# Performance work log

Measured on AMD Instinct MI355X. Metric: run time of the kernel, lower is better.

The kernel has to match this reference:

```python
import jax, jax.numpy as jnp
import numpy as np

D_MODEL = 1024
NHEAD = 16
D_K = D_MODEL // NHEAD
B, S = 4, 2048
LN_EPS = 1e-5


def setup_inputs() -> dict:
    key = jax.random.key(0)
    ks = jax.random.split(key, 12)
    sd = 1.0 / np.sqrt(D_MODEL)
    inp = {
        'x': jax.random.normal(ks[0], (B, S, D_MODEL), dtype=jnp.float32),
        'wq': jax.random.normal(ks[1], (D_MODEL, D_MODEL), dtype=jnp.float32) * sd,
        'bq': jnp.zeros((D_MODEL,), dtype=jnp.float32),
        'wk': jax.random.normal(ks[2], (D_MODEL, D_MODEL), dtype=jnp.float32) * sd,
        'bk': jnp.zeros((D_MODEL,), dtype=jnp.float32),
        'wv': jax.random.normal(ks[3], (D_MODEL, D_MODEL), dtype=jnp.float32) * sd,
        'bv': jnp.zeros((D_MODEL,), dtype=jnp.float32),
        'wo': jax.random.normal(ks[4], (D_MODEL, D_MODEL), dtype=jnp.float32) * sd,
        'bo': jnp.zeros((D_MODEL,), dtype=jnp.float32),
        'conv_w': jax.random.normal(ks[5], (D_MODEL, 3), dtype=jnp.float32) * (1.0 / np.sqrt(3.0)),
        'conv_b': jnp.zeros((D_MODEL,), dtype=jnp.float32),
        'ln_g': jnp.ones((D_MODEL,), dtype=jnp.float32),
        'ln_b': jnp.zeros((D_MODEL,), dtype=jnp.float32),
    }
    return inp


def _forward(x, wq, bq, wk, bk, wv, bv, wo, bo, conv_w, conv_b, ln_g, ln_b):
    b, s, d = x.shape
    # QKV projections -> [B, H, S, Dk]
    q = (x @ wq.T + bq).reshape(b, s, NHEAD, D_K).transpose(0, 2, 1, 3)
    k = (x @ wk.T + bk).reshape(b, s, NHEAD, D_K).transpose(0, 2, 1, 3)
    v = (x @ wv.T + bv).reshape(b, s, NHEAD, D_K).transpose(0, 2, 1, 3)
    # full attention, materialized scores [B, H, S, S]
    scores = jnp.einsum('bhqd,bhkd->bhqk', q, k) / jnp.sqrt(jnp.float32(D_K))
    attn = jax.nn.softmax(scores, axis=-1)  # dropout is identity in eval
    ctx = jnp.einsum('bhqk,bhkd->bhqd', attn, v)
    ctx = ctx.transpose(0, 2, 1, 3).reshape(b, s, d)
    global_attn = ctx @ wo.T + bo
    # depthwise conv1d, kernel 3, padding 1 along sequence
    xp = jnp.pad(x, ((0, 0), (1, 1), (0, 0)))
    local_attn = (xp[:, :-2] * conv_w[:, 0]
                  + xp[:, 1:-1] * conv_w[:, 1]
                  + xp[:, 2:] * conv_w[:, 2]
                  + conv_b)
    combined = global_attn + 0.3 * local_attn
    y = x + combined  # dropout identity in eval
    mu = jnp.mean(y, axis=-1, keepdims=True)
    var = jnp.mean(jnp.square(y - mu), axis=-1, keepdims=True)
    return (y - mu) * jax.lax.rsqrt(var + LN_EPS) * ln_g + ln_b


def reference(x, wq, bq, wk, bk, wv, bv, wo, bo, conv_w, conv_b, ln_g, ln_b):
    return _forward(x, wq, bq, wk, bk, wv, bv, wo, bo, conv_w, conv_b, ln_g, ln_b)
```

## Files before the change

### kernel.cpp

```cpp
#include <hip/hip_runtime.h>

#define DEV __device__ __forceinline__

typedef unsigned short u16;
typedef unsigned int u32;
using f32x4  = __attribute__((ext_vector_type(4))) float;
using f32x16 = __attribute__((ext_vector_type(16))) float;
using s16x8  = __attribute__((ext_vector_type(8))) short;
using u32x2  = __attribute__((ext_vector_type(2))) u32;
using u32x4  = __attribute__((ext_vector_type(4))) u32;
typedef int i32x2 __attribute__((ext_vector_type(2)));

#if __has_builtin(__builtin_amdgcn_exp2f)
#define EXP2(x) __builtin_amdgcn_exp2f(x)
#else
#define EXP2(x) exp2f(x)
#endif

__constant__ const float C2_SCALE = 0.18033688011112042f;
#define S2_SHIFT 17.312340490667560f

DEV u16 f2b(float f) {
  union { float f; u32 u; } v; v.f = f;
  return (u16)((v.u + 0x7FFFu + ((v.u >> 16) & 1u)) >> 16);
}
DEV float b2f(u16 u) {
  union { u32 u; float f; } v; v.u = ((u32)u) << 16;
  return v.f;
}

DEV u32 cvtpk(float lo, float hi) {
  u32 r;
  asm("v_cvt_pk_bf16_f32 %0, %1, %2" : "=v"(r) : "v"(lo), "v"(hi));
  return r;
}

#if __has_builtin(__builtin_amdgcn_permlane32_swap)
DEV void lane32_swap(u32& x, u32& y) {
  i32x2 r = __builtin_amdgcn_permlane32_swap((int)x, (int)y, false, false);
  x = (u32)r[0]; y = (u32)r[1];
}
#else
DEV void lane32_swap(u32& x, u32& y) {
  u32 xo = (u32)__shfl_xor((int)x, 32, 64);
  u32 yo = (u32)__shfl_xor((int)y, 32, 64);
  int hi = (int)((threadIdx.x & 63) >> 5);
  u32 nx = hi ? yo : x;
  u32 ny = hi ? y : xo;
  x = nx; y = ny;
}
#endif

DEV void gload16(const void* g, void* l) {
  __builtin_amdgcn_global_load_lds(
      (const __attribute__((address_space(1))) void*)g,
      (__attribute__((address_space(3))) void*)l, 16, 0, 0);
}

__global__ __launch_bounds__(256) void k_cvt(const float* __restrict__ src,
                                             u16* __restrict__ dst, int n4) {
  int i = blockIdx.x * 256 + threadIdx.x;
  if (i >= n4) return;
  float4 v = ((const float4*)src)[i];
  ushort4 o;
  o.x = f2b(v.x); o.y = f2b(v.y); o.z = f2b(v.z); o.w = f2b(v.w);
  ((ushort4*)dst)[i] = o;
}

__global__ __launch_bounds__(256) void k_cvt_w(
    const float* __restrict__ s0, const float* __restrict__ s1,
    const float* __restrict__ s2, const float* __restrict__ s3,
    u16* __restrict__ dst) {
  int blk = blockIdx.x;
  int widx = blk >> 10;
  int i = (blk & 1023) * 256 + threadIdx.x;
  const float* src = widx == 0 ? s0 : widx == 1 ? s1 : widx == 2 ? s2 : s3;
  float4 v = ((const float4*)src)[i];
  ushort4 o;
  o.x = f2b(v.x); o.y = f2b(v.y); o.z = f2b(v.z); o.w = f2b(v.w);
  ((ushort4*)(dst + (size_t)widx * 1048576))[i] = o;
}

template <int MODE>
__global__ __launch_bounds__(256) void k_gemm_bt(
    const u16* __restrict__ A, const u16* __restrict__ Bw,
    const float* __restrict__ bias0, const float* __restrict__ bias1,
    u16* __restrict__ C, int M, int N, int K) {
  __shared__ alignas(16) u16 lds_[16384];
  char* lds = (char*)lds_;
  const int t = threadIdx.x;
  const int wave = t >> 6, lane = t & 63;
  const int g = lane >> 4, fr = lane & 15;
  const int wr = (wave >> 1) * 64, wc = (wave & 1) * 64;
  const int m0 = blockIdx.y * 128, n0 = blockIdx.x * 128;
  const int chunk = t & 3;

  auto stage = [&](int k0, int buf) {
#pragma unroll
    for (int r = 0; r < 2; ++r) {
      int row = r * 64 + (t >> 2);
      int sw = 8 * (chunk ^ ((row >> 1) & 3));
      char* dst = lds + buf * 16384 + r * 4096 + wave * 1024;
      gload16(A  + (size_t)(m0 + row) * K + k0 + sw, dst);
      gload16(Bw + (size_t)(n0 + row) * K + k0 + sw, dst + 8192);
    }
  };

  f32x4 acc[4][4];
#pragma unroll
  for (int i = 0; i < 4; ++i)
#pragma unroll
    for (int j = 0; j < 4; ++j)
#pragma unroll
      for (int r = 0; r < 4; ++r) acc[i][j][r] = 0.f;

  const int nk = K >> 5;
  stage(0, 0);
  __syncthreads();
  for (int kt = 0; kt < nk; ++kt) {
    const int cur = kt & 1;
    if (kt + 1 < nk) stage((kt + 1) << 5, cur ^ 1);
    s16x8 af[4], bf4[4];
#pragma unroll
    for (int i = 0; i < 4; ++i) {
      int row = wr + i * 16 + fr;
      af[i] = *(const s16x8*)(lds + cur * 16384 + row * 64 +
                              ((g * 16) ^ ((((row >> 1) & 3)) << 4)));
    }
#pragma unroll
    for (int j = 0; j < 4; ++j) {
      int row = wc + j * 16 + fr;
      bf4[j] = *(const s16x8*)(lds + cur * 16384 + 8192 + row * 64 +
                               ((g * 16) ^ ((((row >> 1) & 3)) << 4)));
    }
    __builtin_amdgcn_s_setprio(1);
#pragma unroll
    for (int i = 0; i < 4; ++i)
#pragma unroll
      for (int j = 0; j < 4; ++j)
        acc[i][j] = __builtin_amdgcn_mfma_f32_16x16x32_bf16(af[i], bf4[j], acc[i][j], 0, 0, 0);
    __builtin_amdgcn_s_setprio(0);
    __syncthreads();
  }
#pragma unroll
  for (int j = 0; j < 4; ++j) {
    const int coltile = n0 + wc + j * 16;
    float sc = 1.f;
    const float* bp = bias0;
    if constexpr (MODE == 2) {
      if (coltile >= 1024) { bp = bias1 - 1024; sc = C2_SCALE; }
    }
#pragma unroll
    for (int i = 0; i < 4; ++i)
#pragma unroll
      for (int r = 0; r < 4; ++r) {
        int row = m0 + wr + i * 16 + g * 4 + r;
        int col = coltile + fr;
        float v;
        if constexpr (MODE == 1) v = acc[i][j][r] + bias0[row];
        else                     v = (acc[i][j][r] + bp[col]) * sc;
        C[(size_t)row * N + col] = f2b(v);
      }
  }
}

__global__ __launch_bounds__(256, 2) void k_attn(
    const u16* __restrict__ qkb, const u16* __restrict__ vtb,
    u16* __restrict__ ctx) {
  __shared__ alignas(16) u16 smem_[16384];
  char* smem = (char*)smem_;
  const int bh = blockIdx.x;
  const int b = bh >> 4, h = bh & 15;
  const int qblk = blockIdx.y;
  const int t = threadIdx.x, w = t >> 6, lane = t & 63;
  const int l31 = lane & 31, hi = lane >> 5;
  const int hc = h * 64;
  const int q0 = qblk * 256 + w * 64;

  s16x8 qf[2][4];
#pragma unroll
  for (int s = 0; s < 2; ++s) {
    const u16* qrow = qkb + (size_t)(b * 2048 + q0 + s * 32 + l31) * 2048 + hc + hi * 8;
#pragma unroll
    for (int ks = 0; ks < 4; ++ks) qf[s][ks] = *(const s16x8*)(qrow + ks * 16);
  }

  const u16* kbase  = qkb + (size_t)(b * 2048) * 2048 + 1024 + hc;
  const u16* vtbase = vtb + (size_t)hc * 8192 + b * 2048;

  const int lrow = lane >> 3, seg = lane & 7;
  auto stage = [&](int kt, int buf) {
    const int k0 = kt * 64;
#pragma unroll
    for (int r = 0; r < 2; ++r) {
      int row = r * 32 + w * 8 + lrow;
      int sw = 8 * (seg ^ (row & 7));
      char* dst = smem + buf * 16384 + r * 4096 + w * 1024;
      gload16(kbase  + (size_t)(k0 + row) * 2048 + sw, dst);
      gload16(vtbase + (size_t)row * 8192 + k0 + sw, dst + 8192);
    }
  };

  f32x16 octx[2][2], ns2;
#pragma unroll
  for (int r = 0; r < 16; ++r) {
    octx[0][0][r] = 0.f; octx[0][1][r] = 0.f;
    octx[1][0][r] = 0.f; octx[1][1][r] = 0.f;
    ns2[r] = -S2_SHIFT;
  }
  float lrun[2] = {0.f, 0.f};

  stage(0, 0);
  __syncthreads();
  for (int kt = 0; kt < 32; ++kt) {
    const int cur = kt & 1;
    if (kt + 1 < 32) stage(kt + 1, cur ^ 1);

    f32x16 st[2][2];
    __builtin_amdgcn_s_setprio(1);
#pragma unroll
    for (int ks = 0; ks < 4; ++ks) {
#pragma unroll
      for (int tt = 0; tt < 2; ++tt) {
        int row = tt * 32 + l31;
        s16x8 kf = *(const s16x8*)(smem + cur * 16384 + row * 128 +
                                   ((ks * 32 + hi * 16) ^ ((row & 7) << 4)));
#pragma unroll
        for (int s = 0; s < 2; ++s)
          st[s][tt] = __builtin_amdgcn_mfma_f32_32x32x16_bf16(
              kf, qf[s][ks], ks == 0 ? ns2 : st[s][tt], 0, 0, 0);
      }
    }
    __builtin_amdgcn_s_setprio(0);

    s16x8 pf[2][4];
#pragma unroll
    for (int s = 0; s < 2; ++s) {
      float sm = 0.f;
#pragma unroll
      for (int ks = 0; ks < 4; ++ks) {
        const int tt = ks >> 1, base = (ks & 1) * 8;
        float e[8];
#pragma unroll
        for (int j = 0; j < 8; ++j) {
          e[j] = EXP2(st[s][tt][base + j]);
          sm += e[j];
        }
        u32 u0 = cvtpk(e[0], e[1]), u1 = cvtpk(e[2], e[3]);
        u32 v0 = cvtpk(e[4], e[5]), v1 = cvtpk(e[6], e[7]);
        lane32_swap(u0, v0);
        lane32_swap(u1, v1);
        u32x4 f; f[0] = u0; f[1] = u1; f[2] = v0; f[3] = v1;
        pf[s][ks] = __builtin_bit_cast(s16x8, f);
      }
      lrun[s] += sm;
    }

    __builtin_amdgcn_s_setprio(1);
#pragma unroll
    for (int dt = 0; dt < 2; ++dt)
#pragma unroll
      for (int ks = 0; ks < 4; ++ks) {
        int row = dt * 32 + l31;
        s16x8 vf = *(const s16x8*)(smem + cur * 16384 + 8192 + row * 128 +
                                   ((ks * 32 + hi * 16) ^ ((row & 7) << 4)));
        octx[0][dt] = __builtin_amdgcn_mfma_f32_32x32x16_bf16(vf, pf[0][ks], octx[0][dt], 0, 0, 0);
        octx[1][dt] = __builtin_amdgcn_mfma_f32_32x32x16_bf16(vf, pf[1][ks], octx[1][dt], 0, 0, 0);
      }
    __builtin_amdgcn_s_setprio(0);
    __syncthreads();
  }

  float linv[2];
#pragma unroll
  for (int s = 0; s < 2; ++s) {
    u32 ua = __builtin_bit_cast(u32, lrun[s]), va = ua;
    lane32_swap(ua, va);
    linv[s] = 1.0f / (__builtin_bit_cast(float, ua) + __builtin_bit_cast(float, va));
  }

#pragma unroll
  for (int s = 0; s < 2; ++s) {
    const int ql = w * 64 + s * 32 + l31;
#pragma unroll
    for (int dt = 0; dt < 2; ++dt)
#pragma unroll
      for (int rq = 0; rq < 4; ++rq) {
        int d0 = 8 * rq + 4 * hi + 32 * dt;
        u32x2 pk;
        pk[0] = cvtpk(octx[s][dt][4 * rq + 0] * linv[s], octx[s][dt][4 * rq + 1] * linv[s]);
        pk[1] = cvtpk(octx[s][dt][4 * rq + 2] * linv[s], octx[s][dt][4 * rq + 3] * linv[s]);
        *(u32x2*)(smem + ql * 128 + ((2 * d0) ^ ((ql & 7) << 4))) = pk;
      }
  }
  __syncthreads();
  {
    int qr = t;
    u16* dst = ctx + (size_t)(b * 2048 + qblk * 256 + qr) * 1024 + hc;
#pragma unroll
    for (int i = 0; i < 8; ++i) {
      s16x8 v = *(const s16x8*)(smem + qr * 128 + ((i * 16) ^ ((qr & 7) << 4)));
      *(s16x8*)(dst + i * 8) = v;
    }
  }
}

__global__ __launch_bounds__(256) void k_epi(
    const float* __restrict__ x, const u16* __restrict__ gab,
    const float* __restrict__ cw, const float* __restrict__ cb,
    const float* __restrict__ lg, const float* __restrict__ lb,
    float* __restrict__ out) {
  __shared__ float red[4];
  const int n = ((blockIdx.x & 7) << 10) | (blockIdx.x >> 3);
  const int s = n & 2047;
  const int t = threadIdx.x;
  const int d0 = t * 4;
  const float* xr = x + (size_t)n * 1024;

  float xc[4], xm[4], xp[4];
  { float4 v = *(const float4*)(xr + d0); xc[0]=v.x; xc[1]=v.y; xc[2]=v.z; xc[3]=v.w; }
  if (s > 0) { float4 v = *(const float4*)(xr - 1024 + d0); xm[0]=v.x; xm[1]=v.y; xm[2]=v.z; xm[3]=v.w; }
  else { xm[0]=xm[1]=xm[2]=xm[3]=0.f; }
  if (s < 2047) { float4 v = *(const float4*)(xr + 1024 + d0); xp[0]=v.x; xp[1]=v.y; xp[2]=v.z; xp[3]=v.w; }
  else { xp[0]=xp[1]=xp[2]=xp[3]=0.f; }
  ushort4 gv = *(const ushort4*)(gab + (size_t)n * 1024 + d0);
  float ga4[4] = { b2f(gv.x), b2f(gv.y), b2f(gv.z), b2f(gv.w) };

  float y[4];
#pragma unroll
  for (int i = 0; i < 4; ++i) {
    int d = d0 + i;
    float lo = xm[i] * cw[d * 3] + xc[i] * cw[d * 3 + 1] + xp[i] * cw[d * 3 + 2] + cb[d];
    y[i] = xc[i] + ga4[i] + 0.3f * lo;
  }

  float sm = y[0] + y[1] + y[2] + y[3];
#pragma unroll
  for (int off = 32; off >= 1; off >>= 1) sm += __shfl_xor(sm, off, 64);
  if ((t & 63) == 0) red[t >> 6] = sm;
  __syncthreads();
  float mu = (red[0] + red[1] + red[2] + red[3]) * (1.f / 1024.f);
  __syncthreads();

  float vs = 0.f;
#pragma unroll
  for (int i = 0; i < 4; ++i) { float dd = y[i] - mu; vs += dd * dd; }
#pragma unroll
  for (int off = 32; off >= 1; off >>= 1) vs += __shfl_xor(vs, off, 64);
  if ((t & 63) == 0) red[t >> 6] = vs;
  __syncthreads();
  float var = (red[0] + red[1] + red[2] + red[3]) * (1.f / 1024.f);
  float rs = rsqrtf(var + 1e-5f);
#pragma unroll
  for (int i = 0; i < 4; ++i) {
    int d = d0 + i;
    out[(size_t)n * 1024 + d] = (y[i] - mu) * rs * lg[d] + lb[d];
  }
}

extern "C" void kernel_launch(void* const* d_in, const int* in_sizes, int n_in,
                              void* d_out, int out_size, void* d_ws, size_t ws_size,
                              hipStream_t stream) {
  const float* x  = (const float*)d_in[0];
  const float* wq = (const float*)d_in[1];
  const float* bq = (const float*)d_in[2];
  const float* wk = (const float*)d_in[3];
  const float* bk = (const float*)d_in[4];
  const float* wv = (const float*)d_in[5];
  const float* bv = (const float*)d_in[6];
  const float* wo = (const float*)d_in[7];
  const float* bo = (const float*)d_in[8];
  const float* cw = (const float*)d_in[9];
  const float* cb = (const float*)d_in[10];
  const float* lg = (const float*)d_in[11];
  const float* lb = (const float*)d_in[12];
  float* out = (float*)d_out;

  char* ws = (char*)d_ws;
  const size_t MB = 1ull << 20;
  u16* xb  = (u16*)(ws + 0);
  u16* wqb = (u16*)(ws + 16 * MB);
  u16* wkb = (u16*)(ws + 18 * MB);
  u16* wvb = (u16*)(ws + 20 * MB);
  u16* wob = (u16*)(ws + 22 * MB);
  u16* qkb = (u16*)(ws + 24 * MB);
  u16* vtb = (u16*)(ws + 56 * MB);
  u16* ctx = xb;
  u16* gab = qkb;

  k_cvt<<<8192, 256, 0, stream>>>(x, xb, 2097152);
  k_cvt_w<<<4096, 256, 0, stream>>>(wq, wk, wv, wo, wqb);

  k_gemm_bt<2><<<dim3(16, 64), 256, 0, stream>>>(xb, wqb, bq, bk, qkb, 8192, 2048, 1024);
  k_gemm_bt<1><<<dim3(64, 8), 256, 0, stream>>>(wvb, xb, bv, nullptr, vtb, 1024, 8192, 1024);

  k_attn<<<dim3(64, 8), 256, 0, stream>>>(qkb, vtb, ctx);

  k_gemm_bt<0><<<dim3(8, 64), 256, 0, stream>>>(ctx, wob, bo, nullptr, gab, 8192, 1024, 1024);

  k_epi<<<8192, 256, 0, stream>>>(x, gab, cw, cb, lg, lb, out);
}
```

Before: 200.6 us.

## Add 256x256-tile 8-wave GEMM with chunked staging for fused QK projection

```diff
diff --git a/kernel.cpp b/kernel.cpp
--- a/kernel.cpp
+++ b/kernel.cpp
@@ -16,6 +16,10 @@
 #else
 #define EXP2(x) exp2f(x)
 #endif
+
+#define WAITV(N) asm volatile("s_waitcnt vmcnt(" #N ")" ::: "memory")
+#define LGKM0 do { asm volatile("s_waitcnt lgkmcnt(0)" ::: "memory"); \
+                   __builtin_amdgcn_sched_barrier(0); } while (0)
 
 __constant__ const float C2_SCALE = 0.18033688011112042f;
 #define S2_SHIFT 17.312340490667560f
@@ -81,11 +85,129 @@
   ((ushort4*)(dst + (size_t)widx * 1048576))[i] = o;
 }
 
+#define QUAD(QA, QB)                                                          \
+  do {                                                                        \
+    _Pragma("unroll")                                                         \
+    for (int kk = 0; kk < 2; ++kk)                                            \
+      _Pragma("unroll")                                                       \
+      for (int f = 0; f < 4; ++f)                                             \
+        _Pragma("unroll")                                                     \
+        for (int j = 0; j < 2; ++j)                                           \
+          acc[(QA)*4 + f][(QB)*2 + j] = __builtin_amdgcn_mfma_f32_16x16x32_bf16( \
+              af[f][kk], bf[(QB)*2 + j][kk], acc[(QA)*4 + f][(QB)*2 + j], 0, 0, 0); \
+  } while (0)
+
+__global__ __launch_bounds__(512, 2) void k_gemm8(
+    const u16* __restrict__ A, const u16* __restrict__ Bw,
+    const float* __restrict__ bq, const float* __restrict__ bk,
+    u16* __restrict__ C, int M, int N, int K) {
+  __shared__ alignas(16) u16 lds_[65536];
+  char* lds = (char*)lds_;
+  const int t = threadIdx.x;
+  const int wave = t >> 6, lane = t & 63;
+  const int g = lane >> 4, fr = lane & 15;
+  const int wm = wave >> 2, wn = wave & 3;
+  const int m0 = blockIdx.y * 256, n0 = blockIdx.x * 256;
+  const int seg = t & 7, trow = t >> 3;
+
+  auto stage_chunk = [&](int kt, int buf, int chunk) {
+    const int k0 = kt << 6;
+    const u16* src = (chunk < 2) ? A : Bw;
+    const int isB = chunk >> 1, half = chunk & 1;
+    const int gbase = (isB ? n0 : m0) + half * 128;
+    char* dbase = lds + buf * 65536 + isB * 32768 + half * 16384 + wave * 1024;
+#pragma unroll
+    for (int r = 0; r < 2; ++r) {
+      int rowc = r * 64 + trow;
+      gload16(src + (size_t)(gbase + rowc) * K + k0 + 8 * (seg ^ (rowc & 7)),
+              dbase + r * 8192);
+    }
+  };
+
+  f32x4 acc[8][4];
+#pragma unroll
+  for (int i = 0; i < 8; ++i)
+#pragma unroll
+    for (int j = 0; j < 4; ++j)
+#pragma unroll
+      for (int r = 0; r < 4; ++r) acc[i][j][r] = 0.f;
+
+  s16x8 af[4][2], bf[4][2];
+  const int nk = K >> 6;
+
+  stage_chunk(0, 0, 0); stage_chunk(0, 0, 1);
+  stage_chunk(0, 0, 2); stage_chunk(0, 0, 3);
+
+  for (int kt = 0; kt < nk; ++kt) {
+    const int cur = kt & 1, nxt = cur ^ 1;
+    const bool more = (kt + 1 < nk);
+    const char* ab = lds + cur * 65536;
+    const char* bb = lds + cur * 65536 + 32768;
+
+    auto lda = [&](int f, int kk) -> s16x8 {
+      int row = wm * 128 + f * 16 + fr;
+      return *(const s16x8*)(ab + row * 128 + ((kk * 64 + g * 16) ^ ((row & 7) << 4)));
+    };
+    auto ldb = [&](int j, int kk) -> s16x8 {
+      int row = wn * 64 + j * 16 + fr;
+      return *(const s16x8*)(bb + row * 128 + ((kk * 64 + g * 16) ^ ((row & 7) << 4)));
+    };
+
+    if (more) { stage_chunk(kt + 1, nxt, 0); WAITV(2); } else WAITV(0);
+    __builtin_amdgcn_s_barrier();
+    __builtin_amdgcn_sched_barrier(0);
+#pragma unroll
+    for (int f = 0; f < 4; ++f) { af[f][0] = lda(f, 0); af[f][1] = lda(f, 1); }
+#pragma unroll
+    for (int j = 0; j < 2; ++j) { bf[j][0] = ldb(j, 0); bf[j][1] = ldb(j, 1); }
+    LGKM0;
+    __builtin_amdgcn_s_setprio(1); QUAD(0, 0); __builtin_amdgcn_s_setprio(0);
+    __builtin_amdgcn_s_barrier();
+
+#pragma unroll
+    for (int j = 2; j < 4; ++j) { bf[j][0] = ldb(j, 0); bf[j][1] = ldb(j, 1); }
+    if (more) stage_chunk(kt + 1, nxt, 1);
+    __builtin_amdgcn_s_barrier();
+    LGKM0;
+    __builtin_amdgcn_s_setprio(1); QUAD(0, 1); __builtin_amdgcn_s_setprio(0);
+    __builtin_amdgcn_s_barrier();
+
+#pragma unroll
+    for (int f = 0; f < 4; ++f) { af[f][0] = lda(f + 4, 0); af[f][1] = lda(f + 4, 1); }
+    if (more) stage_chunk(kt + 1, nxt, 2);
+    __builtin_amdgcn_s_barrier();
+    LGKM0;
+    __builtin_amdgcn_s_setprio(1); QUAD(1, 1); __builtin_amdgcn_s_setprio(0);
+    __builtin_amdgcn_s_barrier();
+
+    if (more) stage_chunk(kt + 1, nxt, 3);
+    __builtin_amdgcn_s_barrier();
+    __builtin_amdgcn_s_setprio(1); QUAD(1, 0); __builtin_amdgcn_s_setprio(0);
+    __builtin_amdgcn_s_barrier();
+  }
+
+#pragma unroll
+  for (int j = 0; j < 4; ++j) {
+    const int coltile = n0 + wn * 64 + j * 16;
+    const bool isK = coltile >= 1024;
+    const float* bp = isK ? (bk - 1024) : bq;
+    const float sc = isK ? C2_SCALE : 1.f;
+#pragma unroll
+    for (int f = 0; f < 8; ++f)
+#pragma unroll
+      for (int r = 0; r < 4; ++r) {
+        int row = m0 + wm * 128 + f * 16 + g * 4 + r;
+        int col = coltile + fr;
+        C[(size_t)row * N + col] = f2b((acc[f][j][r] + bp[col]) * sc);
+      }
+  }
+}
+
 template <int MODE>
 __global__ __launch_bounds__(256) void k_gemm_bt(
     const u16* __restrict__ A, const u16* __restrict__ Bw,
-    const float* __restrict__ bias0, const float* __restrict__ bias1,
-    u16* __restrict__ C, int M, int N, int K) {
+    const float* __restrict__ bias0, u16* __restrict__ C,
+    int M, int N, int K) {
   __shared__ alignas(16) u16 lds_[16384];
   char* lds = (char*)lds_;
   const int t = threadIdx.x;
@@ -144,21 +266,13 @@
   }
 #pragma unroll
   for (int j = 0; j < 4; ++j) {
-    const int coltile = n0 + wc + j * 16;
-    float sc = 1.f;
-    const float* bp = bias0;
-    if constexpr (MODE == 2) {
-      if (coltile >= 1024) { bp = bias1 - 1024; sc = C2_SCALE; }
-    }
 #pragma unroll
     for (int i = 0; i < 4; ++i)
 #pragma unroll
       for (int r = 0; r < 4; ++r) {
         int row = m0 + wr + i * 16 + g * 4 + r;
-        int col = coltile + fr;
-        float v;
-        if constexpr (MODE == 1) v = acc[i][j][r] + bias0[row];
-        else                     v = (acc[i][j][r] + bp[col]) * sc;
+        int col = n0 + wc + j * 16 + fr;
+        float v = acc[i][j][r] + (MODE == 1 ? bias0[row] : bias0[col]);
         C[(size_t)row * N + col] = f2b(v);
       }
   }
@@ -380,7 +494,6 @@
   const size_t MB = 1ull << 20;
   u16* xb  = (u16*)(ws + 0);
   u16* wqb = (u16*)(ws + 16 * MB);
-  u16* wkb = (u16*)(ws + 18 * MB);
   u16* wvb = (u16*)(ws + 20 * MB);
   u16* wob = (u16*)(ws + 22 * MB);
   u16* qkb = (u16*)(ws + 24 * MB);
@@ -391,12 +504,12 @@
   k_cvt<<<8192, 256, 0, stream>>>(x, xb, 2097152);
   k_cvt_w<<<4096, 256, 0, stream>>>(wq, wk, wv, wo, wqb);
 
-  k_gemm_bt<2><<<dim3(16, 64), 256, 0, stream>>>(xb, wqb, bq, bk, qkb, 8192, 2048, 1024);
-  k_gemm_bt<1><<<dim3(64, 8), 256, 0, stream>>>(wvb, xb, bv, nullptr, vtb, 1024, 8192, 1024);
+  k_gemm8<<<dim3(8, 32), 512, 0, stream>>>(xb, wqb, bq, bk, qkb, 8192, 2048, 1024);
+  k_gemm_bt<1><<<dim3(64, 8), 256, 0, stream>>>(wvb, xb, bv, vtb, 1024, 8192, 1024);
 
   k_attn<<<dim3(64, 8), 256, 0, stream>>>(qkb, vtb, ctx);
 
-  k_gemm_bt<0><<<dim3(8, 64), 256, 0, stream>>>(ctx, wob, bo, nullptr, gab, 8192, 1024, 1024);
+  k_gemm_bt<0><<<dim3(8, 64), 256, 0, stream>>>(ctx, wob, bo, gab, 8192, 1024, 1024);
 
   k_epi<<<8192, 256, 0, stream>>>(x, gab, cw, cb, lg, lb, out);
 }
```

After: 199.5 us. No clear change (-0.5%).
